# Kernel tuning notes

Measured on AMD Instinct MI355X. Metric: run time of the kernel, lower is better.

The kernel has to match this reference:

```python
import jax, jax.numpy as jnp
import numpy as np

K = 20  # n_neighbors

def _edge_features(x, k):
    # x: [B, C, N] -> edge features [B, 2C, N, k] using dynamic kNN graph
    sq = jnp.sum(x * x, axis=1)                          # [B, N]
    inner = jnp.einsum('bcn,bcm->bnm', x, x)             # [B, N, N]
    neg_dist = 2.0 * inner - sq[:, :, None] - sq[:, None, :]
    idx = jax.lax.top_k(neg_dist, k)[1]                  # [B, N, k] nearest neighbors
    # gather neighbor features: xj[b,c,n,j] = x[b,c,idx[b,n,j]]
    xj = jnp.take_along_axis(x[:, :, None, :], idx[:, None, :, :], axis=3)  # [B, C, N, k]
    xi = jnp.broadcast_to(x[:, :, :, None], xj.shape)
    return jnp.concatenate([xj - xi, xi], axis=1)        # [B, 2C, N, k]

def _lrelu(v):
    return jax.nn.leaky_relu(v, 0.2)

def _edge_conv(x, W, b, k):
    f = _edge_features(x, k)                              # [B, 2C, N, k]
    h = jnp.einsum('bcnk,oc->bonk', f, W) + b[None, :, None, None]
    return jnp.max(_lrelu(h), axis=3)                     # [B, O, N]

def setup_inputs() -> dict:
    key = jax.random.key(0)
    ks = jax.random.split(key, 12)
    conv_dims = (64, 64, 128, 256)
    in_dims = (3, 64, 64, 128)
    inp = {'x': jax.random.normal(ks[0], (16, 2048, 3), dtype=jnp.float32)}
    for i, (ci, co) in enumerate(zip(in_dims, conv_dims)):
        s = 1.0 / np.sqrt(2 * ci)
        inp[f'W{i}'] = jax.random.uniform(ks[1 + 2 * i], (co, 2 * ci), jnp.float32, -s, s)
        inp[f'b{i}'] = jax.random.uniform(ks[2 + 2 * i], (co,), jnp.float32, -s, s)
    sf = 1.0 / np.sqrt(sum(conv_dims))
    inp['Wf'] = jax.random.uniform(ks[9], (1024, sum(conv_dims)), jnp.float32, -sf, sf)
    inp['bf'] = jax.random.uniform(ks[10], (1024,), jnp.float32, -sf, sf)
    return inp

def reference(x, W0, b0, W1, b1, W2, b2, W3, b3, Wf, bf):
    h = jnp.transpose(x, (0, 2, 1))                       # [B, 3, N]
    xs = []
    for W, b in ((W0, b0), (W1, b1), (W2, b2), (W3, b3)):
        h = _edge_conv(h, W, b, K)
        xs.append(h)
    h = jnp.concatenate(xs, axis=1)                       # [B, 512, N]
    h = _lrelu(jnp.einsum('bcn,oc->bon', h, Wf) + bf[None, :, None])  # [B, 1024, N]
    return jnp.max(h, axis=2)                             # [B, 1024]
```

## Files before the change

kernel.cpp:

```cpp
#include <hip/hip_runtime.h>
#include <hip/hip_bf16.h>
#include <math.h>

#define NPTS 2048
#define NB 16
#define KNN 20

typedef __attribute__((ext_vector_type(8))) short bf16x8;
typedef __attribute__((ext_vector_type(4))) float f32x4;

__device__ __forceinline__ float lrelu(float v) { return fmaxf(v, 0.2f * v); }

__device__ __forceinline__ void split2(float a, float b, unsigned& hp, unsigned& lp) {
    float2 f2; f2.x = a; f2.y = b;
    __hip_bfloat162 h2 = __float22bfloat162_rn(f2);
    unsigned hb; __builtin_memcpy(&hb, &h2, 4);
    float la = a - __uint_as_float(hb << 16);
    float lb = b - __uint_as_float(hb & 0xFFFF0000u);
    float2 l2; l2.x = la; l2.y = lb;
    __hip_bfloat162 k2 = __float22bfloat162_rn(l2);
    unsigned lb2; __builtin_memcpy(&lb2, &k2, 4);
    hp = hb; lp = lb2;
}

template<int CTRL, int RM>
__device__ __forceinline__ float dpp_fmax_step(float x) {
    int t = __builtin_amdgcn_update_dpp((int)0xFF800000, __float_as_int(x),
                                        CTRL, RM, 0xF, false);
    return fmaxf(x, __int_as_float(t));
}
__device__ __forceinline__ float wave_max_bcast(float x) {
    x = dpp_fmax_step<0x111, 0xF>(x);
    x = dpp_fmax_step<0x112, 0xF>(x);
    x = dpp_fmax_step<0x114, 0xF>(x);
    x = dpp_fmax_step<0x118, 0xF>(x);
    x = dpp_fmax_step<0x142, 0xA>(x);
    x = dpp_fmax_step<0x143, 0xC>(x);
    return __int_as_float(__builtin_amdgcn_readlane(__float_as_int(x), 63));
}

__global__ void transpose_kernel(const float* __restrict__ x, float* __restrict__ h0) {
    int t = blockIdx.x * blockDim.x + threadIdx.x;
    if (t >= NB * NPTS) return;
    int b = t / NPTS, n = t % NPTS;
    const float* src = x + (size_t)t * 3;
    float* dst = h0 + (size_t)b * 3 * NPTS + n;
    dst[0]        = src[0];
    dst[NPTS]     = src[1];
    dst[2 * NPTS] = src[2];
}

template<int C>
__global__ __launch_bounds__(512) void knn_kernel(const float* __restrict__ xin, long bstride,
                                                  int* __restrict__ idxT) {
    __shared__ __align__(16) float dist[8][NPTS];
    int b  = blockIdx.x & 15;
    int qb = blockIdx.x >> 4;
    int tid = threadIdx.x;
    int lane = tid & 63, w = tid >> 6;
    const float* xb = xin + (size_t)b * bstride;
    int m0 = 4 * tid;

    for (int rg = 0; rg < 4; ++rg) {
        int n0 = qb * 32 + rg * 8;
        const float* xq = xb + n0;

        float4 acc[8];
#pragma unroll
        for (int r = 0; r < 8; ++r) acc[r] = make_float4(0.f, 0.f, 0.f, 0.f);
        float4 sn = make_float4(0.f, 0.f, 0.f, 0.f);

#pragma unroll 4
        for (int c = 0; c < C; ++c) {
            const float* rowc = xb + (size_t)c * NPTS;
            float4 xv = *reinterpret_cast<const float4*>(&rowc[m0]);
            float4 q0 = *reinterpret_cast<const float4*>(&xq[(size_t)c * NPTS]);
            float4 q1 = *reinterpret_cast<const float4*>(&xq[(size_t)c * NPTS + 4]);
            sn.x = fmaf(xv.x, xv.x, sn.x);
            sn.y = fmaf(xv.y, xv.y, sn.y);
            sn.z = fmaf(xv.z, xv.z, sn.z);
            sn.w = fmaf(xv.w, xv.w, sn.w);
            float q[8] = {q0.x, q0.y, q0.z, q0.w, q1.x, q1.y, q1.z, q1.w};
#pragma unroll
            for (int r = 0; r < 8; ++r) {
                acc[r].x = fmaf(q[r], xv.x, acc[r].x);
                acc[r].y = fmaf(q[r], xv.y, acc[r].y);
                acc[r].z = fmaf(q[r], xv.z, acc[r].z);
                acc[r].w = fmaf(q[r], xv.w, acc[r].w);
            }
        }
        {
            int p = m0 ^ (((m0 >> 5) & 7) << 2);
#pragma unroll
            for (int r = 0; r < 8; ++r) {
                float4 dv;
                dv.x = 2.f * acc[r].x - sn.x;
                dv.y = 2.f * acc[r].y - sn.y;
                dv.z = 2.f * acc[r].z - sn.z;
                dv.w = 2.f * acc[r].w - sn.w;
                *reinterpret_cast<float4*>(&dist[r][p]) = dv;
            }
        }
        __syncthreads();

        float v[32];
        {
            const float* drow = &dist[w][32 * lane];
            int s = (lane & 7) << 2;
#pragma unroll
            for (int u = 0; u < 8; ++u) {
                float4 t = *reinterpret_cast<const float4*>(&drow[(4 * u) ^ s]);
                v[4 * u + 0] = t.x; v[4 * u + 1] = t.y;
                v[4 * u + 2] = t.z; v[4 * u + 3] = t.w;
            }
        }

        float gm[4]; int gi[4];
#pragma unroll
        for (int g = 0; g < 4; ++g) {
            gm[g] = v[8 * g]; gi[g] = 8 * g;
#pragma unroll
            for (int i = 1; i < 8; ++i)
                if (v[8 * g + i] > gm[g]) { gm[g] = v[8 * g + i]; gi[g] = 8 * g + i; }
        }
        float lv = gm[0]; int lm = gi[0];
#pragma unroll
        for (int g = 1; g < 4; ++g) if (gm[g] > lv) { lv = gm[g]; lm = gi[g]; }

        int rbm = 0;

        for (int j = 0; j < KNN; ++j) {
            float gv = wave_max_bcast(lv);
            unsigned long long mk = __ballot(lv == gv);
            int winner = (int)__builtin_ctzll(mk);
            int wm = __builtin_amdgcn_readlane(lm, winner);
            int bm = winner * 32 + wm;
            rbm = (lane == j) ? bm : rbm;

            bool iswin = (lane == winner);
            int g = wm >> 3, ii = wm & 7;
#pragma unroll
            for (int gq = 0; gq < 4; ++gq) {
                if (gq == g) {
#pragma unroll
                    for (int i = 0; i < 8; ++i)
                        v[8 * gq + i] = (iswin && (ii == i)) ? -INFINITY : v[8 * gq + i];
                    float nm = v[8 * gq]; int ni = 8 * gq;
#pragma unroll
                    for (int i = 1; i < 8; ++i)
                        if (v[8 * gq + i] > nm) { nm = v[8 * gq + i]; ni = 8 * gq + i; }
                    gm[gq] = iswin ? nm : gm[gq];
                    gi[gq] = iswin ? ni : gi[gq];
                }
            }
            lv = gm[0]; lm = gi[0];
#pragma unroll
            for (int g2 = 1; g2 < 4; ++g2) if (gm[g2] > lv) { lv = gm[g2]; lm = gi[g2]; }
        }
        if (lane < KNN) idxT[((size_t)b * KNN + lane) * NPTS + n0 + w] = rbm;

        if (rg < 3) __syncthreads();
    }
}

__global__ void prep_w_kernel(const float* __restrict__ W, int C, int O,
                              float* __restrict__ Wa, float* __restrict__ Wd) {
    int t = blockIdx.x * blockDim.x + threadIdx.x;
    if (t >= C * O) return;
    int c = t / O, o = t % O;
    float a = W[o * 2 * C + c];
    float d = W[o * 2 * C + C + c] - a;
    Wa[c * O + o] = a;
    Wd[c * O + o] = d;
}

__global__ __launch_bounds__(256) void edge_mm_kernel(const float* __restrict__ xin, long bstride,
                                                      int C, int O,
                                                      const float* __restrict__ Wa,
                                                      const float* __restrict__ Wd,
                                                      const float* __restrict__ bias,
                                                      float* __restrict__ y,
                                                      float* __restrict__ base, long base_bstride) {
    int m = blockIdx.x * 256 + threadIdx.x;
    int ngrp = O >> 3;
    int og = blockIdx.y % ngrp, b = blockIdx.y / ngrp;
    int o0 = og * 8;
    const float* xb = xin + (size_t)b * bstride + m;
    float a1[8], a2[8];
#pragma unroll
    for (int i = 0; i < 8; ++i) { a1[i] = 0.f; a2[i] = 0.f; }
#pragma unroll 2
    for (int c = 0; c < C; ++c) {
        float h = xb[(size_t)c * NPTS];
        const float* wa = Wa + c * O + o0;
        const float* wd = Wd + c * O + o0;
#pragma unroll
        for (int i = 0; i < 8; ++i) {
            a1[i] = fmaf(wa[i], h, a1[i]);
            a2[i] = fmaf(wd[i], h, a2[i]);
        }
    }
#pragma unroll
    for (int i = 0; i < 8; ++i) {
        y[((size_t)b * O + o0 + i) * NPTS + m] = a1[i];
        base[(size_t)b * base_bstride + (size_t)(o0 + i) * NPTS + m] = a2[i] + bias[o0 + i];
    }
}

__global__ __launch_bounds__(256) void gather_max_kernel(const float* __restrict__ y, int O,
                                                         const int* __restrict__ idxT,
                                                         float* __restrict__ feat_slice,
                                                         long bstride) {
    __shared__ float yrow[NPTS];
    int b = blockIdx.x & 15, o = blockIdx.x >> 4;
    const float* ysrc = y + ((size_t)b * O + o) * NPTS;
    for (int m = threadIdx.x; m < NPTS; m += 256) yrow[m] = ysrc[m];
    __syncthreads();
    float* fs = feat_slice + (size_t)b * bstride + (size_t)o * NPTS;
    const int* ib = idxT + (size_t)b * KNN * NPTS;
    for (int s = 0; s < 8; ++s) {
        int n = threadIdx.x + 256 * s;
        float mx = -INFINITY;
#pragma unroll
        for (int j = 0; j < KNN; ++j) mx = fmaxf(mx, yrow[ib[(size_t)j * NPTS + n]]);
        fs[n] = lrelu(mx + fs[n]);
    }
}

__global__ void wf_split_kernel(const float* __restrict__ Wf,
                                unsigned* __restrict__ Wfh, unsigned* __restrict__ Wfl) {
    int t = blockIdx.x * 256 + threadIdx.x;
    if (t >= 262144) return;
    unsigned h, l;
    split2(Wf[2 * t], Wf[2 * t + 1], h, l);
    Wfh[t] = h; Wfl[t] = l;
}

#define GP 40
__global__ __launch_bounds__(256) void final_gemm_mfma(
    const float* __restrict__ feat,
    const unsigned short* __restrict__ Wfh,
    const unsigned short* __restrict__ Wfl,
    float* __restrict__ pmax) {
    __shared__ __align__(16) unsigned short Ah[128 * GP];
    __shared__ __align__(16) unsigned short Al[128 * GP];
    __shared__ __align__(16) unsigned short Bh[128 * GP];
    __shared__ __align__(16) unsigned short Bl[128 * GP];

    int ot = blockIdx.x, nt = blockIdx.y, b = blockIdx.z;
    int o0 = ot * 128, n0 = nt * 128;
    int tid = threadIdx.x;
    int lane = tid & 63, w = tid >> 6;
    int wm = w & 1, wn = w >> 1;
    int l15 = lane & 15, q = lane >> 4;

    f32x4 acc[4][4];
#pragma unroll
    for (int mi = 0; mi < 4; ++mi)
#pragma unroll
        for (int ni = 0; ni < 4; ++ni) acc[mi][ni] = (f32x4)0.f;

    const float* fb = feat + (size_t)b * 512 * NPTS;
    int bn = tid & 127, kh = tid >> 7;

    for (int c0 = 0; c0 < 512; c0 += 32) {
#pragma unroll
        for (int p = 0; p < 2; ++p) {
            int e = p * 256 + tid;
            int r = e >> 2, qq = e & 3;
            size_t go = (size_t)(o0 + r) * 512 + c0 + qq * 8;
            *(uint4*)&Ah[r * GP + qq * 8] = *(const uint4*)(Wfh + go);
            *(uint4*)&Al[r * GP + qq * 8] = *(const uint4*)(Wfl + go);
        }
        {
            const float* src = fb + (size_t)(c0 + kh * 16) * NPTS + n0 + bn;
            float v[16];
#pragma unroll
            for (int j = 0; j < 16; ++j) v[j] = src[(size_t)j * NPTS];
            unsigned hw[8], lw[8];
#pragma unroll
            for (int p = 0; p < 8; ++p) split2(v[2 * p], v[2 * p + 1], hw[p], lw[p]);
            unsigned short* bh = &Bh[bn * GP + kh * 16];
            unsigned short* bl = &Bl[bn * GP + kh * 16];
            *(uint4*)(bh)     = make_uint4(hw[0], hw[1], hw[2], hw[3]);
            *(uint4*)(bh + 8) = make_uint4(hw[4], hw[5], hw[6], hw[7]);
            *(uint4*)(bl)     = make_uint4(lw[0], lw[1], lw[2], lw[3]);
            *(uint4*)(bl + 8) = make_uint4(lw[4], lw[5], lw[6], lw[7]);
        }
        __syncthreads();

        bf16x8 bhf[4], blf[4];
#pragma unroll
        for (int ni = 0; ni < 4; ++ni) {
            int row = wn * 64 + ni * 16 + l15;
            bhf[ni] = *(const bf16x8*)&Bh[row * GP + q * 8];
            blf[ni] = *(const bf16x8*)&Bl[row * GP + q * 8];
        }
#pragma unroll
        for (int mi = 0; mi < 4; ++mi) {
            int row = wm * 64 + mi * 16 + l15;
            bf16x8 ah = *(const bf16x8*)&Ah[row * GP + q * 8];
            bf16x8 al = *(const bf16x8*)&Al[row * GP + q * 8];
#pragma unroll
            for (int ni = 0; ni < 4; ++ni) {
                acc[mi][ni] = __builtin_amdgcn_mfma_f32_16x16x32_bf16(ah, bhf[ni], acc[mi][ni], 0, 0, 0);
                acc[mi][ni] = __builtin_amdgcn_mfma_f32_16x16x32_bf16(ah, blf[ni], acc[mi][ni], 0, 0, 0);
                acc[mi][ni] = __builtin_amdgcn_mfma_f32_16x16x32_bf16(al, bhf[ni], acc[mi][ni], 0, 0, 0);
            }
        }
        __syncthreads();
    }

    int slot = nt * 2 + wn;
#pragma unroll
    for (int mi = 0; mi < 4; ++mi) {
        float m4[4];
#pragma unroll
        for (int r = 0; r < 4; ++r) {
            float m = acc[mi][0][r];
            m = fmaxf(m, acc[mi][1][r]);
            m = fmaxf(m, acc[mi][2][r]);
            m = fmaxf(m, acc[mi][3][r]);
            m4[r] = m;
        }
#pragma unroll
        for (int off = 1; off < 16; off <<= 1) {
#pragma unroll
            for (int r = 0; r < 4; ++r)
                m4[r] = fmaxf(m4[r], __shfl_xor(m4[r], off, 16));
        }
        if (l15 == 0) {
            int mbase = o0 + wm * 64 + mi * 16 + q * 4;
#pragma unroll
            for (int r = 0; r < 4; ++r)
                pmax[((size_t)b * 1024 + mbase + r) * 32 + slot] = m4[r];
        }
    }
}

__global__ void final_reduce_kernel(const float* __restrict__ pmax,
                                    const float* __restrict__ bf,
                                    float* __restrict__ out) {
    int t = blockIdx.x * blockDim.x + threadIdx.x;
    if (t >= NB * 1024) return;
    const float* p = pmax + (size_t)t * 32;
    float m = p[0];
#pragma unroll
    for (int i = 1; i < 32; ++i) m = fmaxf(m, p[i]);
    out[t] = lrelu(m + bf[t & 1023]);
}

extern "C" void kernel_launch(void* const* d_in, const int* in_sizes, int n_in,
                              void* d_out, int out_size, void* d_ws, size_t ws_size,
                              hipStream_t stream) {
    const float* x  = (const float*)d_in[0];
    const float* W[4]  = {(const float*)d_in[1], (const float*)d_in[3],
                          (const float*)d_in[5], (const float*)d_in[7]};
    const float* bb[4] = {(const float*)d_in[2], (const float*)d_in[4],
                          (const float*)d_in[6], (const float*)d_in[8]};
    const float* Wf = (const float*)d_in[9];
    const float* bf = (const float*)d_in[10];
    float* out = (float*)d_out;

    float* ws   = (float*)d_ws;
    float* h0   = ws;
    int*   idxT = (int*)(ws + 98304 + 32768);
    float* y    = (float*)(idxT + 655360);
    float* feat = y + 8388608;
    float* Wa   = feat + 16777216 + 262144;
    float* Wd   = Wa + 32768;

    unsigned* Wfh = (unsigned*)y;
    unsigned* Wfl = (unsigned*)(y + 262144);
    float*    pmax = y + 524288;

    transpose_kernel<<<128, 256, 0, stream>>>(x, h0);

    const int  Cs[4]   = {3, 64, 64, 128};
    const int  Os[4]   = {64, 64, 128, 256};
    const int  offs[4] = {0, 64, 128, 256};

    for (int l = 0; l < 4; ++l) {
        const float* in = (l == 0) ? h0 : feat + (size_t)offs[l - 1] * NPTS;
        long bstr = (l == 0) ? (long)3 * NPTS : (long)512 * NPTS;
        int C = Cs[l], O = Os[l];

        int kb = (NPTS / 32) * NB;
        if (C == 3)       knn_kernel<3>  <<<kb, 512, 0, stream>>>(in, bstr, idxT);
        else if (C == 64) knn_kernel<64> <<<kb, 512, 0, stream>>>(in, bstr, idxT);
        else              knn_kernel<128><<<kb, 512, 0, stream>>>(in, bstr, idxT);

        prep_w_kernel<<<(C * O + 255) / 256, 256, 0, stream>>>(W[l], C, O, Wa, Wd);

        float* fslice = feat + (size_t)offs[l] * NPTS;
        edge_mm_kernel<<<dim3(NPTS / 256, NB * (O >> 3)), 256, 0, stream>>>(
            in, bstr, C, O, Wa, Wd, bb[l], y, fslice, (long)512 * NPTS);

        gather_max_kernel<<<O * NB, 256, 0, stream>>>(y, O, idxT, fslice, (long)512 * NPTS);
    }

    wf_split_kernel<<<1024, 256, 0, stream>>>(Wf, Wfh, Wfl);
    final_gemm_mfma<<<dim3(8, 16, NB), 256, 0, stream>>>(
        feat, (const unsigned short*)Wfh, (const unsigned short*)Wfl, pmax);
    final_reduce_kernel<<<64, 256, 0, stream>>>(pmax, bf, out);
}
```

Measured before the change: 1.113 ms.

## Reuse kNN indices across 8 output channels in gather-max; compute norms once

The gather-max kernel now has each block load 8 output-channel rows of y into shared memory and process half of the points. Each neighbor index read from global memory is therefore reused for 8 channels, where before it was re-read for every channel. Separately, the kNN kernel computes the candidate squared norms only on the first row group and reuses them for the remaining three. The gather kernel now uses 64KB of shared memory per block, which may reduce occupancy.

Result: no change. 1.116 ms (+0.3%).

```diff
diff --git a/kernel.cpp b/kernel.cpp
--- a/kernel.cpp
+++ b/kernel.cpp
@@ -60,6 +60,7 @@
     int lane = tid & 63, w = tid >> 6;
     const float* xb = xin + (size_t)b * bstride;
     int m0 = 4 * tid;
+    float4 sn = make_float4(0.f, 0.f, 0.f, 0.f);
 
     for (int rg = 0; rg < 4; ++rg) {
         int n0 = qb * 32 + rg * 8;
@@ -68,25 +69,42 @@
         float4 acc[8];
 #pragma unroll
         for (int r = 0; r < 8; ++r) acc[r] = make_float4(0.f, 0.f, 0.f, 0.f);
-        float4 sn = make_float4(0.f, 0.f, 0.f, 0.f);
-
+
+        if (rg == 0) {
 #pragma unroll 4
-        for (int c = 0; c < C; ++c) {
-            const float* rowc = xb + (size_t)c * NPTS;
-            float4 xv = *reinterpret_cast<const float4*>(&rowc[m0]);
-            float4 q0 = *reinterpret_cast<const float4*>(&xq[(size_t)c * NPTS]);
-            float4 q1 = *reinterpret_cast<const float4*>(&xq[(size_t)c * NPTS + 4]);
-            sn.x = fmaf(xv.x, xv.x, sn.x);
-            sn.y = fmaf(xv.y, xv.y, sn.y);
-            sn.z = fmaf(xv.z, xv.z, sn.z);
-            sn.w = fmaf(xv.w, xv.w, sn.w);
-            float q[8] = {q0.x, q0.y, q0.z, q0.w, q1.x, q1.y, q1.z, q1.w};
-#pragma unroll
-            for (int r = 0; r < 8; ++r) {
-                acc[r].x = fmaf(q[r], xv.x, acc[r].x);
-                acc[r].y = fmaf(q[r], xv.y, acc[r].y);
-                acc[r].z = fmaf(q[r], xv.z, acc[r].z);
-                acc[r].w = fmaf(q[r], xv.w, acc[r].w);
+            for (int c = 0; c < C; ++c) {
+                const float* rowc = xb + (size_t)c * NPTS;
+                float4 xv = *reinterpret_cast<const float4*>(&rowc[m0]);
+                float4 q0 = *reinterpret_cast<const float4*>(&xq[(size_t)c * NPTS]);
+                float4 q1 = *reinterpret_cast<const float4*>(&xq[(size_t)c * NPTS + 4]);
+                sn.x = fmaf(xv.x, xv.x, sn.x);
+                sn.y = fmaf(xv.y, xv.y, sn.y);
+                sn.z = fmaf(xv.z, xv.z, sn.z);
+                sn.w = fmaf(xv.w, xv.w, sn.w);
+                float q[8] = {q0.x, q0.y, q0.z, q0.w, q1.x, q1.y, q1.z, q1.w};
+#pragma unroll
+                for (int r = 0; r < 8; ++r) {
+                    acc[r].x = fmaf(q[r], xv.x, acc[r].x);
+                    acc[r].y = fmaf(q[r], xv.y, acc[r].y);
+                    acc[r].z = fmaf(q[r], xv.z, acc[r].z);
+                    acc[r].w = fmaf(q[r], xv.w, acc[r].w);
+                }
+            }
+        } else {
+#pragma unroll 4
+            for (int c = 0; c < C; ++c) {
+                const float* rowc = xb + (size_t)c * NPTS;
+                float4 xv = *reinterpret_cast<const float4*>(&rowc[m0]);
+                float4 q0 = *reinterpret_cast<const float4*>(&xq[(size_t)c * NPTS]);
+                float4 q1 = *reinterpret_cast<const float4*>(&xq[(size_t)c * NPTS + 4]);
+                float q[8] = {q0.x, q0.y, q0.z, q0.w, q1.x, q1.y, q1.z, q1.w};
+#pragma unroll
+                for (int r = 0; r < 8; ++r) {
+                    acc[r].x = fmaf(q[r], xv.x, acc[r].x);
+                    acc[r].y = fmaf(q[r], xv.y, acc[r].y);
+                    acc[r].z = fmaf(q[r], xv.z, acc[r].z);
+                    acc[r].w = fmaf(q[r], xv.w, acc[r].w);
+                }
             }
         }
         {
@@ -211,19 +229,38 @@
                                                          const int* __restrict__ idxT,
                                                          float* __restrict__ feat_slice,
                                                          long bstride) {
-    __shared__ float yrow[NPTS];
-    int b = blockIdx.x & 15, o = blockIdx.x >> 4;
-    const float* ysrc = y + ((size_t)b * O + o) * NPTS;
-    for (int m = threadIdx.x; m < NPTS; m += 256) yrow[m] = ysrc[m];
+    __shared__ __align__(16) float yrow[8][NPTS];
+    int b  = blockIdx.x & 15;
+    int nc = (blockIdx.x >> 4) & 1;
+    int og = blockIdx.x >> 5;
+    int o0 = og * 8;
+    const float* ysrc = y + ((size_t)b * O + o0) * NPTS;
+    for (int e = threadIdx.x; e < 8 * (NPTS / 4); e += 256) {
+        int i = e >> 9;
+        int m4 = e & 511;
+        *reinterpret_cast<float4*>(&yrow[i][4 * m4]) =
+            *reinterpret_cast<const float4*>(&ysrc[(size_t)i * NPTS + 4 * m4]);
+    }
     __syncthreads();
-    float* fs = feat_slice + (size_t)b * bstride + (size_t)o * NPTS;
-    const int* ib = idxT + (size_t)b * KNN * NPTS;
-    for (int s = 0; s < 8; ++s) {
+    float* fs = feat_slice + (size_t)b * bstride + (size_t)o0 * NPTS;
+    const int* ib = idxT + (size_t)b * KNN * NPTS + nc * (NPTS / 2);
+    for (int s = 0; s < 4; ++s) {
         int n = threadIdx.x + 256 * s;
-        float mx = -INFINITY;
-#pragma unroll
-        for (int j = 0; j < KNN; ++j) mx = fmaxf(mx, yrow[ib[(size_t)j * NPTS + n]]);
-        fs[n] = lrelu(mx + fs[n]);
+        int gn = nc * (NPTS / 2) + n;
+        float mx[8];
+#pragma unroll
+        for (int i = 0; i < 8; ++i) mx[i] = -INFINITY;
+#pragma unroll 4
+        for (int j = 0; j < KNN; ++j) {
+            int id = ib[(size_t)j * NPTS + n];
+#pragma unroll
+            for (int i = 0; i < 8; ++i) mx[i] = fmaxf(mx[i], yrow[i][id]);
+        }
+#pragma unroll
+        for (int i = 0; i < 8; ++i) {
+            float* fp = fs + (size_t)i * NPTS + gn;
+            *fp = lrelu(mx[i] + *fp);
+        }
     }
 }
 
@@ -396,7 +433,8 @@
         edge_mm_kernel<<<dim3(NPTS / 256, NB * (O >> 3)), 256, 0, stream>>>(
             in, bstr, C, O, Wa, Wd, bb[l], y, fslice, (long)512 * NPTS);
 
-        gather_max_kernel<<<O * NB, 256, 0, stream>>>(y, O, idxT, fslice, (long)512 * NPTS);
+        gather_max_kernel<<<(O / 8) * 2 * NB, 256, 0, stream>>>(
+            y, O, idxT, fslice, (long)512 * NPTS);
     }
 
     wf_split_kernel<<<1024, 256, 0, stream>>>(Wf, Wfh, Wfl);
```
